# Kernel tuning notes

Hardware: AMD Instinct MI355X
Metric: run time of the kernel (lower is better)

The kernel has to match this reference:

```python
import jax, jax.numpy as jnp
import numpy as np

N_NODES = 50000
N_EDGES = 1600000
IN_DIM = 128
HEADS = 4
HID = 16
NEG_SLOPE = 0.2  # DGL GATConv default


def setup_inputs() -> dict:
    key = jax.random.key(0)
    ks = jax.random.split(key, 7)
    features = jax.random.normal(ks[0], (N_NODES, IN_DIM), dtype=jnp.float32)
    W = jax.random.normal(ks[1], (IN_DIM, HEADS * HID), dtype=jnp.float32) * 0.1
    attn_l = jax.random.normal(ks[2], (HEADS, HID), dtype=jnp.float32) * 0.1
    attn_r = jax.random.normal(ks[3], (HEADS, HID), dtype=jnp.float32) * 0.1
    bias = jax.random.normal(ks[4], (HEADS * HID,), dtype=jnp.float32) * 0.1
    src = jax.random.randint(ks[5], (N_EDGES,), 0, N_NODES, dtype=jnp.int64)
    dst = jax.random.randint(ks[6], (N_EDGES,), 0, N_NODES, dtype=jnp.int64)
    return {"features": features, "W": W, "attn_l": attn_l, "attn_r": attn_r,
            "bias": bias, "src": src, "dst": dst}


def reference(features, W, attn_l, attn_r, bias, src, dst):
    N = features.shape[0]
    H, D = attn_l.shape
    # linear projection -> per-head features [N, H, D]
    feat = (features @ W).reshape(N, H, D)
    el = jnp.einsum('nhd,hd->nh', feat, attn_l)  # [N, H]
    er = jnp.einsum('nhd,hd->nh', feat, attn_r)  # [N, H]
    # per-edge unnormalized attention logits [E, H]
    e = jax.nn.leaky_relu(el[src] + er[dst], negative_slope=NEG_SLOPE)
    # edge softmax segmented by destination node (numerically stable)
    emax = jax.ops.segment_max(e, dst, num_segments=N)
    ee = jnp.exp(e - emax[dst])
    denom = jax.ops.segment_sum(ee, dst, num_segments=N)
    alpha = ee / denom[dst]  # [E, H]
    # weighted neighbor aggregation: scatter-add of alpha * feat[src]
    msg = feat[src] * alpha[:, :, None]  # [E, H, D]
    out = jax.ops.segment_sum(msg, dst, num_segments=N)  # [N, H, D]
    out = out + bias.reshape(1, H, D)
    # wrapper GAT.forward averages over heads
    return out.mean(axis=1)  # [N, D]
```

## Files before the change

### kernel.cpp

```cpp
#include <hip/hip_runtime.h>
#include <hip/hip_bf16.h>

#define IN_DIM 128
#define HEADS 4
#define HID 16
#define HD 64
#define NEG_SLOPE 0.2f
#define PSHIFT 7
#define PCAP 5120
#define NPMAX 512
#define EPB 8192
#define NB_PROJ 256
#define NTILE 5

typedef __attribute__((ext_vector_type(8))) short bf16x8;
typedef __attribute__((ext_vector_type(4))) float f32x4;

__device__ __forceinline__ float lrelu_exp(float x) {
    float e = x > 0.0f ? x : NEG_SLOPE * x;
    return __expf(e);
}

__device__ __forceinline__ unsigned short f2bf(float x) {
    unsigned int u = __float_as_uint(x);
    return (unsigned short)((u + 0x7fffu + ((u >> 16) & 1u)) >> 16);
}

__global__ __launch_bounds__(256) void k_prjpart(const float* __restrict__ features,
                                                 const float* __restrict__ W,
                                                 const float* __restrict__ attn_l,
                                                 const float* __restrict__ attn_r,
                                                 __hip_bfloat16* __restrict__ feat16,
                                                 float* __restrict__ el,
                                                 float* __restrict__ er,
                                                 const int* __restrict__ src,
                                                 const int* __restrict__ dst,
                                                 int* __restrict__ cursor,
                                                 unsigned int* __restrict__ partbuf,
                                                 int n_nodes, int n_edges,
                                                 int npart, int npartblk) {
    __shared__ float smem[IN_DIM * HD];

    if (blockIdx.x < (unsigned)npartblk) {
        int* hist = (int*)smem;
        int* base = (int*)smem + NPMAX;
        const int t = threadIdx.x;
        for (int i = t; i < npart; i += 256) hist[i] = 0;
        __syncthreads();

        const int e0 = blockIdx.x * EPB;
        unsigned int vals[32];
#pragma unroll
        for (int j = 0; j < 8; ++j) {
            int e = e0 + j * 1024 + t * 4;
            if (e + 4 <= n_edges) {
                int4 s4 = *reinterpret_cast<const int4*>(src + e);
                int4 d4 = *reinterpret_cast<const int4*>(dst + e);
                vals[j * 4 + 0] = ((unsigned)d4.x << 16) | (unsigned)s4.x;
                vals[j * 4 + 1] = ((unsigned)d4.y << 16) | (unsigned)s4.y;
                vals[j * 4 + 2] = ((unsigned)d4.z << 16) | (unsigned)s4.z;
                vals[j * 4 + 3] = ((unsigned)d4.w << 16) | (unsigned)s4.w;
            } else {
#pragma unroll
                for (int k = 0; k < 4; ++k) {
                    int ee = e + k;
                    vals[j * 4 + k] = (ee < n_edges)
                        ? (((unsigned)dst[ee] << 16) | (unsigned)src[ee])
                        : 0xffffffffu;
                }
            }
        }
#pragma unroll
        for (int j = 0; j < 32; ++j)
            if (vals[j] != 0xffffffffu) atomicAdd(&hist[vals[j] >> (16 + PSHIFT)], 1);
        __syncthreads();
        for (int i = t; i < npart; i += 256) {
            base[i] = atomicAdd(&cursor[i], hist[i]);
            hist[i] = 0;
        }
        __syncthreads();
#pragma unroll
        for (int j = 0; j < 32; ++j) {
            unsigned int v = vals[j];
            if (v != 0xffffffffu) {
                int p = v >> (16 + PSHIFT);
                int idx = base[p] + atomicAdd(&hist[p], 1);
                if (idx < PCAP) partbuf[(size_t)p * PCAP + idx] = v;
            }
        }
        return;
    }

    for (int i = threadIdx.x; i < IN_DIM * HD; i += 256) smem[i] = W[i];
    __syncthreads();

    uint4 ent[NTILE];
#pragma unroll
    for (int i = 0; i < NTILE; ++i) {
        const int e  = threadIdx.x + (i << 8);
        const int fi = e >> 6;
        const int ln = e & 63;
        const int c  = fi >> 2;
        const int q  = fi & 3;
        const int colid = ln & 15;
        const int quad  = ln >> 4;
        unsigned short v[8];
        if (c < 4) {
#pragma unroll
            for (int j = 0; j < 8; ++j) {
                int k = q * 32 + quad * 8 + j;
                v[j] = f2bf(smem[k * HD + c * 16 + colid]);
            }
        } else if (colid < 8) {
            const int h = colid & 3;
            const float* attn = (colid < 4) ? attn_l : attn_r;
            float at[16];
#pragma unroll
            for (int d = 0; d < 16; ++d) at[d] = attn[h * 16 + d];
#pragma unroll
            for (int j = 0; j < 8; ++j) {
                int k = q * 32 + quad * 8 + j;
                float sum = 0.f;
#pragma unroll
                for (int d = 0; d < 16; ++d)
                    sum = fmaf(smem[k * HD + h * 16 + d], at[d], sum);
                v[j] = f2bf(sum);
            }
        } else {
#pragma unroll
            for (int j = 0; j < 8; ++j) v[j] = 0;
        }
        ent[i].x = (unsigned int)v[0] | ((unsigned int)v[1] << 16);
        ent[i].y = (unsigned int)v[2] | ((unsigned int)v[3] << 16);
        ent[i].z = (unsigned int)v[4] | ((unsigned int)v[5] << 16);
        ent[i].w = (unsigned int)v[6] | ((unsigned int)v[7] << 16);
    }
    __syncthreads();

    uint4* fragw = (uint4*)smem;
#pragma unroll
    for (int i = 0; i < NTILE; ++i)
        fragw[threadIdx.x + (i << 8)] = ent[i];
    __syncthreads();

    const bf16x8* frags = (const bf16x8*)smem;
    const int lane  = threadIdx.x & 63;
    const int wave  = threadIdx.x >> 6;
    const int colid = lane & 15;
    const int quad  = lane >> 4;

    const int ngroups = (n_nodes + 15) >> 4;
    const int gwave = (blockIdx.x - npartblk) * 4 + wave;
    const int nwaves = NB_PROJ * 4;

    int g = gwave;
    float4 ra[8];
    if (g < ngroups) {
        int rown = g * 16 + colid;
        if (rown >= n_nodes) rown = n_nodes - 1;
        const float* fp = features + (size_t)rown * IN_DIM + quad * 8;
#pragma unroll
        for (int q = 0; q < 4; ++q) {
            ra[q * 2]     = *reinterpret_cast<const float4*>(fp + q * 32);
            ra[q * 2 + 1] = *reinterpret_cast<const float4*>(fp + q * 32 + 4);
        }
    }

    while (g < ngroups) {
        const int gn = g + nwaves;
        float4 rb[8];
        if (gn < ngroups) {
            int rown = gn * 16 + colid;
            if (rown >= n_nodes) rown = n_nodes - 1;
            const float* fp = features + (size_t)rown * IN_DIM + quad * 8;
#pragma unroll
            for (int q = 0; q < 4; ++q) {
                rb[q * 2]     = *reinterpret_cast<const float4*>(fp + q * 32);
                rb[q * 2 + 1] = *reinterpret_cast<const float4*>(fp + q * 32 + 4);
            }
        }

        const int n0 = g * 16;
        f32x4 acc[NTILE];
#pragma unroll
        for (int c = 0; c < NTILE; ++c) acc[c] = (f32x4){0.f, 0.f, 0.f, 0.f};

#pragma unroll
        for (int q = 0; q < 4; ++q) {
            float4 a0 = ra[q * 2];
            float4 a1 = ra[q * 2 + 1];
            bf16x8 av;
            av[0] = (short)f2bf(a0.x); av[1] = (short)f2bf(a0.y);
            av[2] = (short)f2bf(a0.z); av[3] = (short)f2bf(a0.w);
            av[4] = (short)f2bf(a1.x); av[5] = (short)f2bf(a1.y);
            av[6] = (short)f2bf(a1.z); av[7] = (short)f2bf(a1.w);
#pragma unroll
            for (int c = 0; c < NTILE; ++c) {
                bf16x8 bv = frags[(c * 4 + q) * 64 + lane];
                acc[c] = __builtin_amdgcn_mfma_f32_16x16x32_bf16(av, bv, acc[c], 0, 0, 0);
            }
        }

        const bool full = (n0 + 16 <= n_nodes);
#pragma unroll
        for (int c = 0; c < 4; ++c) {
#pragma unroll
            for (int r = 0; r < 4; ++r) {
                int n = n0 + quad * 4 + r;
                if (full || n < n_nodes) {
                    ((unsigned short*)feat16)[(size_t)n * HD + c * 16 + colid] = f2bf(acc[c][r]);
                }
            }
        }
        if (colid < 8) {
            float* dstp = (colid < 4) ? el : er;
            const int h = colid & 3;
#pragma unroll
            for (int r = 0; r < 4; ++r) {
                int n = n0 + quad * 4 + r;
                if (full || n < n_nodes) {
                    dstp[(size_t)n * HEADS + h] = acc[4][r];
                }
            }
        }

#pragma unroll
        for (int j = 0; j < 8; ++j) ra[j] = rb[j];
        g = gn;
    }
}

__global__ __launch_bounds__(512) void k_sort(const unsigned int* __restrict__ partbuf,
                                              const int* __restrict__ cursor,
                                              unsigned short* __restrict__ csr,
                                              int* __restrict__ row_ptr,
                                              unsigned short* __restrict__ deg16,
                                              int n_nodes) {
    __shared__ int hist[128];
    __shared__ int scan_s[128];
    const int p = blockIdx.x;
    const int t = threadIdx.x;
    const int count = min(cursor[p], PCAP);
    const unsigned int* buf = partbuf + (size_t)p * PCAP;

    unsigned int vals[10];
#pragma unroll
    for (int j = 0; j < 10; ++j) {
        int i = t + j * 512;
        vals[j] = (i < count) ? buf[i] : 0xffffffffu;
    }

    if (t < 128) hist[t] = 0;
    __syncthreads();
#pragma unroll
    for (int j = 0; j < 10; ++j)
        if (vals[j] != 0xffffffffu) atomicAdd(&hist[(vals[j] >> 16) & 127], 1);
    __syncthreads();

    int v = 0;
    if (t < 128) {
        v = hist[t];
        scan_s[t] = v;
    }
    __syncthreads();
    for (int off = 1; off < 128; off <<= 1) {
        int u = (t >= off && t < 128) ? scan_s[t - off] : 0;
        __syncthreads();
        if (t < 128) scan_s[t] += u;
        __syncthreads();
    }
    if (t < 128) {
        const int excl = scan_s[t] - v;
        const int node = (p << PSHIFT) + t;
        if (node < n_nodes) {
            row_ptr[node] = p * PCAP + excl;
            deg16[node] = (unsigned short)v;
        }
        hist[t] = excl;
    }
    __syncthreads();
    unsigned short* cbase = csr + (size_t)p * PCAP;
#pragma unroll
    for (int j = 0; j < 10; ++j) {
        unsigned int val = vals[j];
        if (val != 0xffffffffu) {
            int ld = (val >> 16) & 127;
            int pos = atomicAdd(&hist[ld], 1);
            cbase[pos] = (unsigned short)(val & 0xffffu);
        }
    }
}

__global__ __launch_bounds__(256) void k_agg(const int* __restrict__ row_ptr,
                                             const unsigned short* __restrict__ deg16,
                                             const unsigned short* __restrict__ csr,
                                             const float* __restrict__ el,
                                             const float* __restrict__ er,
                                             const unsigned int* __restrict__ feat16u,
                                             const float* __restrict__ bias,
                                             float* __restrict__ out,
                                             int n_nodes) {
    int n = (blockIdx.x * blockDim.x + threadIdx.x) >> 6;
    if (n >= n_nodes) return;
    const int lane = threadIdx.x & 63;
    const int half = lane >> 5;
    const int sub = lane & 31;
    const int h = sub >> 3;
    const int eW = lane >> 2;
    const int hW = lane & 3;

    const int beg = row_ptr[n];
    const int deg = (int)deg16[n];
    const unsigned short* row = csr + beg;
    const float erW = er[(size_t)n * HEADS + hW];

    const int baseLane = half * 4 + h;

    float nx0 = 0.f, ny0 = 0.f, nx1 = 0.f, ny1 = 0.f;
    float denacc = 0.f;

    bool valid = (eW < deg);
    int s = valid ? (int)row[eW] : 0;
    float w = valid ? lrelu_exp(el[(size_t)s * HEADS + hW] + erW) : 0.f;

    for (int i0 = 0; i0 < deg; i0 += 16) {
        denacc += w;
        const unsigned int pw = ((unsigned int)f2bf(w) << 16) | (unsigned int)s;

        unsigned int pk[8];
#pragma unroll
        for (int j = 0; j < 8; ++j) pk[j] = __shfl(pw, baseLane + (j << 3));

        const bool v2 = (i0 + 16 + eW < deg);
        int s2 = v2 ? (int)row[i0 + 16 + eW] : 0;

        unsigned int pf[8];
#pragma unroll
        for (int j = 0; j < 8; ++j)
            pf[j] = feat16u[((pk[j] & 0xffffu) << 5) + sub];

        float w2 = v2 ? lrelu_exp(el[(size_t)s2 * HEADS + hW] + erW) : 0.f;

#pragma unroll
        for (int j = 0; j < 8; ++j) {
            float wj = __uint_as_float(pk[j] & 0xffff0000u);
            if (j & 1) {
                nx1 = fmaf(wj, __uint_as_float(pf[j] << 16), nx1);
                ny1 = fmaf(wj, __uint_as_float(pf[j] & 0xffff0000u), ny1);
            } else {
                nx0 = fmaf(wj, __uint_as_float(pf[j] << 16), nx0);
                ny0 = fmaf(wj, __uint_as_float(pf[j] & 0xffff0000u), ny0);
            }
        }
        s = s2;
        w = w2;
    }

    float den = denacc;
    den += __shfl_xor(den, 4);
    den += __shfl_xor(den, 8);
    den += __shfl_xor(den, 16);
    den += __shfl_xor(den, 32);
    float denh = __shfl(den, h);

    float nx = nx0 + nx1, ny = ny0 + ny1;
    nx += __shfl_xor(nx, 32);
    ny += __shfl_xor(ny, 32);
    float inv = (denh > 0.f) ? 0.25f / denh : 0.f;
    float rx = nx * inv;
    float ry = ny * inv;
    rx += __shfl_xor(rx, 8);
    ry += __shfl_xor(ry, 8);
    rx += __shfl_xor(rx, 16);
    ry += __shfl_xor(ry, 16);
    if (lane < 8) {
        int dp = lane;
        float bx = 0.25f * (bias[2 * dp] + bias[HID + 2 * dp] +
                            bias[2 * HID + 2 * dp] + bias[3 * HID + 2 * dp]);
        float by = 0.25f * (bias[2 * dp + 1] + bias[HID + 2 * dp + 1] +
                            bias[2 * HID + 2 * dp + 1] + bias[3 * HID + 2 * dp + 1]);
        *reinterpret_cast<float2*>(out + (size_t)n * HID + 2 * dp) =
            make_float2(rx + bx, ry + by);
    }
}

extern "C" void kernel_launch(void* const* d_in, const int* in_sizes, int n_in,
                              void* d_out, int out_size, void* d_ws, size_t ws_size,
                              hipStream_t stream) {
    const float* features = (const float*)d_in[0];
    const float* W        = (const float*)d_in[1];
    const float* attn_l   = (const float*)d_in[2];
    const float* attn_r   = (const float*)d_in[3];
    const float* bias     = (const float*)d_in[4];
    const int*   src      = (const int*)d_in[5];
    const int*   dst      = (const int*)d_in[6];
    float* out = (float*)d_out;

    const int n_nodes = in_sizes[0] / IN_DIM;
    const int n_edges = in_sizes[5];
    const int npart = (n_nodes + (1 << PSHIFT) - 1) >> PSHIFT;
    const int npartblk = (n_edges + EPB - 1) / EPB;

    char* ws = (char*)d_ws;
    __hip_bfloat16* feat16 = (__hip_bfloat16*)ws; ws += (size_t)n_nodes * HD * sizeof(__hip_bfloat16);
    float* el      = (float*)ws;                  ws += (size_t)n_nodes * HEADS * sizeof(float);
    float* er      = (float*)ws;                  ws += (size_t)n_nodes * HEADS * sizeof(float);
    unsigned int* partbuf = (unsigned int*)ws;    ws += (size_t)npart * PCAP * sizeof(unsigned int);
    unsigned short* csr = (unsigned short*)ws;    ws += (size_t)npart * PCAP * sizeof(unsigned short);
    int* row_ptr   = (int*)ws;                    ws += (size_t)n_nodes * sizeof(int);
    unsigned short* deg16 = (unsigned short*)ws;  ws += (size_t)n_nodes * sizeof(unsigned short);
    int* cursor    = (int*)ws;                    ws += NPMAX * sizeof(int);

    hipMemsetAsync(cursor, 0, NPMAX * sizeof(int), stream);

    k_prjpart<<<npartblk + NB_PROJ, 256, 0, stream>>>(features, W, attn_l, attn_r,
                                                      feat16, el, er, src, dst,
                                                      cursor, partbuf,
                                                      n_nodes, n_edges, npart, npartblk);
    k_sort<<<npart, 512, 0, stream>>>(partbuf, cursor, csr, row_ptr, deg16, n_nodes);
    k_agg<<<(n_nodes + 3) / 4, 256, 0, stream>>>(row_ptr, deg16, csr, el, er,
                                                 (const unsigned int*)feat16, bias, out, n_nodes);
}
```

Baseline: 151.4 us.

## Fuse per-partition sort and aggregation into one kernel using shared-memory CSR

Merges the counting-sort kernel and the aggregation kernel. Each partition block builds its CSR slice in LDS, then its 8 waves each aggregate 16 destination nodes from that local slice. This removes the global CSR, row_ptr and degree buffers and one kernel launch. In exchange, the aggregation phase runs with only one block per 128-node partition and each wave handles its nodes serially, which reduces the parallelism available to hide gather latency.

```diff
diff --git a/kernel.cpp b/kernel.cpp
--- a/kernel.cpp
+++ b/kernel.cpp
@@ -230,14 +230,19 @@
     }
 }
 
-__global__ __launch_bounds__(512) void k_sort(const unsigned int* __restrict__ partbuf,
-                                              const int* __restrict__ cursor,
-                                              unsigned short* __restrict__ csr,
-                                              int* __restrict__ row_ptr,
-                                              unsigned short* __restrict__ deg16,
-                                              int n_nodes) {
+__global__ __launch_bounds__(512) void k_sortagg(const unsigned int* __restrict__ partbuf,
+                                                 const int* __restrict__ cursor,
+                                                 const float* __restrict__ el,
+                                                 const float* __restrict__ er,
+                                                 const unsigned int* __restrict__ feat16u,
+                                                 const float* __restrict__ bias,
+                                                 float* __restrict__ out,
+                                                 int n_nodes) {
+    __shared__ unsigned short csr_l[PCAP];
     __shared__ int hist[128];
-    __shared__ int scan_s[128];
+    __shared__ int rowbeg[128];
+    __shared__ int rowdeg[128];
+
     const int p = blockIdx.x;
     const int t = threadIdx.x;
     const int count = min(cursor[p], PCAP);
@@ -260,127 +265,117 @@
     int v = 0;
     if (t < 128) {
         v = hist[t];
-        scan_s[t] = v;
+        rowbeg[t] = v;
     }
     __syncthreads();
     for (int off = 1; off < 128; off <<= 1) {
-        int u = (t >= off && t < 128) ? scan_s[t - off] : 0;
+        int u = (t >= off && t < 128) ? rowbeg[t - off] : 0;
         __syncthreads();
-        if (t < 128) scan_s[t] += u;
+        if (t < 128) rowbeg[t] += u;
         __syncthreads();
     }
     if (t < 128) {
-        const int excl = scan_s[t] - v;
-        const int node = (p << PSHIFT) + t;
-        if (node < n_nodes) {
-            row_ptr[node] = p * PCAP + excl;
-            deg16[node] = (unsigned short)v;
-        }
+        const int excl = rowbeg[t] - v;
+        rowbeg[t] = excl;
+        rowdeg[t] = v;
         hist[t] = excl;
     }
     __syncthreads();
-    unsigned short* cbase = csr + (size_t)p * PCAP;
 #pragma unroll
     for (int j = 0; j < 10; ++j) {
         unsigned int val = vals[j];
         if (val != 0xffffffffu) {
             int ld = (val >> 16) & 127;
             int pos = atomicAdd(&hist[ld], 1);
-            cbase[pos] = (unsigned short)(val & 0xffffu);
-        }
-    }
-}
-
-__global__ __launch_bounds__(256) void k_agg(const int* __restrict__ row_ptr,
-                                             const unsigned short* __restrict__ deg16,
-                                             const unsigned short* __restrict__ csr,
-                                             const float* __restrict__ el,
-                                             const float* __restrict__ er,
-                                             const unsigned int* __restrict__ feat16u,
-                                             const float* __restrict__ bias,
-                                             float* __restrict__ out,
-                                             int n_nodes) {
-    int n = (blockIdx.x * blockDim.x + threadIdx.x) >> 6;
-    if (n >= n_nodes) return;
-    const int lane = threadIdx.x & 63;
+            csr_l[pos] = (unsigned short)(val & 0xffffu);
+        }
+    }
+    __syncthreads();
+
+    const int wave = t >> 6;
+    const int lane = t & 63;
     const int half = lane >> 5;
     const int sub = lane & 31;
     const int h = sub >> 3;
     const int eW = lane >> 2;
     const int hW = lane & 3;
-
-    const int beg = row_ptr[n];
-    const int deg = (int)deg16[n];
-    const unsigned short* row = csr + beg;
-    const float erW = er[(size_t)n * HEADS + hW];
-
     const int baseLane = half * 4 + h;
 
-    float nx0 = 0.f, ny0 = 0.f, nx1 = 0.f, ny1 = 0.f;
-    float denacc = 0.f;
-
-    bool valid = (eW < deg);
-    int s = valid ? (int)row[eW] : 0;
-    float w = valid ? lrelu_exp(el[(size_t)s * HEADS + hW] + erW) : 0.f;
-
-    for (int i0 = 0; i0 < deg; i0 += 16) {
-        denacc += w;
-        const unsigned int pw = ((unsigned int)f2bf(w) << 16) | (unsigned int)s;
-
-        unsigned int pk[8];
-#pragma unroll
-        for (int j = 0; j < 8; ++j) pk[j] = __shfl(pw, baseLane + (j << 3));
-
-        const bool v2 = (i0 + 16 + eW < deg);
-        int s2 = v2 ? (int)row[i0 + 16 + eW] : 0;
-
-        unsigned int pf[8];
-#pragma unroll
-        for (int j = 0; j < 8; ++j)
-            pf[j] = feat16u[((pk[j] & 0xffffu) << 5) + sub];
-
-        float w2 = v2 ? lrelu_exp(el[(size_t)s2 * HEADS + hW] + erW) : 0.f;
-
-#pragma unroll
-        for (int j = 0; j < 8; ++j) {
-            float wj = __uint_as_float(pk[j] & 0xffff0000u);
-            if (j & 1) {
-                nx1 = fmaf(wj, __uint_as_float(pf[j] << 16), nx1);
-                ny1 = fmaf(wj, __uint_as_float(pf[j] & 0xffff0000u), ny1);
-            } else {
-                nx0 = fmaf(wj, __uint_as_float(pf[j] << 16), nx0);
-                ny0 = fmaf(wj, __uint_as_float(pf[j] & 0xffff0000u), ny0);
-            }
-        }
-        s = s2;
-        w = w2;
-    }
-
-    float den = denacc;
-    den += __shfl_xor(den, 4);
-    den += __shfl_xor(den, 8);
-    den += __shfl_xor(den, 16);
-    den += __shfl_xor(den, 32);
-    float denh = __shfl(den, h);
-
-    float nx = nx0 + nx1, ny = ny0 + ny1;
-    nx += __shfl_xor(nx, 32);
-    ny += __shfl_xor(ny, 32);
-    float inv = (denh > 0.f) ? 0.25f / denh : 0.f;
-    float rx = nx * inv;
-    float ry = ny * inv;
-    rx += __shfl_xor(rx, 8);
-    ry += __shfl_xor(ry, 8);
-    rx += __shfl_xor(rx, 16);
-    ry += __shfl_xor(ry, 16);
-    if (lane < 8) {
-        int dp = lane;
-        float bx = 0.25f * (bias[2 * dp] + bias[HID + 2 * dp] +
-                            bias[2 * HID + 2 * dp] + bias[3 * HID + 2 * dp]);
-        float by = 0.25f * (bias[2 * dp + 1] + bias[HID + 2 * dp + 1] +
-                            bias[2 * HID + 2 * dp + 1] + bias[3 * HID + 2 * dp + 1]);
-        *reinterpret_cast<float2*>(out + (size_t)n * HID + 2 * dp) =
-            make_float2(rx + bx, ry + by);
+    for (int i = 0; i < 16; ++i) {
+        const int ln = wave * 16 + i;
+        const int n = (p << PSHIFT) + ln;
+        if (n >= n_nodes) break;
+
+        const int beg = rowbeg[ln];
+        const int deg = rowdeg[ln];
+        const float erW = er[(size_t)n * HEADS + hW];
+
+        float nx0 = 0.f, ny0 = 0.f, nx1 = 0.f, ny1 = 0.f;
+        float denacc = 0.f;
+
+        bool valid = (eW < deg);
+        int s = valid ? (int)csr_l[beg + eW] : 0;
+        float w = valid ? lrelu_exp(el[(size_t)s * HEADS + hW] + erW) : 0.f;
+
+        for (int i0 = 0; i0 < deg; i0 += 16) {
+            denacc += w;
+            const unsigned int pw = ((unsigned int)f2bf(w) << 16) | (unsigned int)s;
+
+            unsigned int pk[8];
+#pragma unroll
+            for (int j = 0; j < 8; ++j) pk[j] = __shfl(pw, baseLane + (j << 3));
+
+            const bool v2 = (i0 + 16 + eW < deg);
+            int s2 = v2 ? (int)csr_l[beg + i0 + 16 + eW] : 0;
+
+            unsigned int pf[8];
+#pragma unroll
+            for (int j = 0; j < 8; ++j)
+                pf[j] = feat16u[((pk[j] & 0xffffu) << 5) + sub];
+
+            float w2 = v2 ? lrelu_exp(el[(size_t)s2 * HEADS + hW] + erW) : 0.f;
+
+#pragma unroll
+            for (int j = 0; j < 8; ++j) {
+                float wj = __uint_as_float(pk[j] & 0xffff0000u);
+                if (j & 1) {
+                    nx1 = fmaf(wj, __uint_as_float(pf[j] << 16), nx1);
+                    ny1 = fmaf(wj, __uint_as_float(pf[j] & 0xffff0000u), ny1);
+                } else {
+                    nx0 = fmaf(wj, __uint_as_float(pf[j] << 16), nx0);
+                    ny0 = fmaf(wj, __uint_as_float(pf[j] & 0xffff0000u), ny0);
+                }
+            }
+            s = s2;
+            w = w2;
+        }
+
+        float den = denacc;
+        den += __shfl_xor(den, 4);
+        den += __shfl_xor(den, 8);
+        den += __shfl_xor(den, 16);
+        den += __shfl_xor(den, 32);
+        float denh = __shfl(den, h);
+
+        float nx = nx0 + nx1, ny = ny0 + ny1;
+        nx += __shfl_xor(nx, 32);
+        ny += __shfl_xor(ny, 32);
+        float inv = (denh > 0.f) ? 0.25f / denh : 0.f;
+        float rx = nx * inv;
+        float ry = ny * inv;
+        rx += __shfl_xor(rx, 8);
+        ry += __shfl_xor(ry, 8);
+        rx += __shfl_xor(rx, 16);
+        ry += __shfl_xor(ry, 16);
+        if (lane < 8) {
+            int dp = lane;
+            float bx = 0.25f * (bias[2 * dp] + bias[HID + 2 * dp] +
+                                bias[2 * HID + 2 * dp] + bias[3 * HID + 2 * dp]);
+            float by = 0.25f * (bias[2 * dp + 1] + bias[HID + 2 * dp + 1] +
+                                bias[2 * HID + 2 * dp + 1] + bias[3 * HID + 2 * dp + 1]);
+            *reinterpret_cast<float2*>(out + (size_t)n * HID + 2 * dp) =
+                make_float2(rx + bx, ry + by);
+        }
     }
 }
 
@@ -406,9 +401,6 @@
     float* el      = (float*)ws;                  ws += (size_t)n_nodes * HEADS * sizeof(float);
     float* er      = (float*)ws;                  ws += (size_t)n_nodes * HEADS * sizeof(float);
     unsigned int* partbuf = (unsigned int*)ws;    ws += (size_t)npart * PCAP * sizeof(unsigned int);
-    unsigned short* csr = (unsigned short*)ws;    ws += (size_t)npart * PCAP * sizeof(unsigned short);
-    int* row_ptr   = (int*)ws;                    ws += (size_t)n_nodes * sizeof(int);
-    unsigned short* deg16 = (unsigned short*)ws;  ws += (size_t)n_nodes * sizeof(unsigned short);
     int* cursor    = (int*)ws;                    ws += NPMAX * sizeof(int);
 
     hipMemsetAsync(cursor, 0, NPMAX * sizeof(int), stream);
@@ -417,7 +409,6 @@
                                                       feat16, el, er, src, dst,
                                                       cursor, partbuf,
                                                       n_nodes, n_edges, npart, npartblk);
-    k_sort<<<npart, 512, 0, stream>>>(partbuf, cursor, csr, row_ptr, deg16, n_nodes);
-    k_agg<<<(n_nodes + 3) / 4, 256, 0, stream>>>(row_ptr, deg16, csr, el, er,
-                                                 (const unsigned int*)feat16, bias, out, n_nodes);
+    k_sortagg<<<npart, 512, 0, stream>>>(partbuf, cursor, el, er,
+                                         (const unsigned int*)feat16, bias, out, n_nodes);
 }
```

Measured after the change: 156.8 us. +3.5%, slower.
